# Performance work log

Measured on AMD Instinct MI355X. Metric: run time of the kernel, lower is better.

Reference implementation:

```python
import jax, jax.numpy as jnp
import numpy as np
from jax import lax

B, T, I, H = 4096, 128, 16, 64


def setup_inputs() -> dict:
    key = jax.random.key(0)
    ks = jax.random.split(key, 7)
    s_ih = 1.0 / np.sqrt(H)
    return {
        "x": jax.random.normal(ks[0], (B, T, I), dtype=jnp.float32),
        "w_ih": jax.random.uniform(ks[1], (3 * H, I), jnp.float32, -s_ih, s_ih),
        "w_hh": jax.random.uniform(ks[2], (3 * H, H), jnp.float32, -s_ih, s_ih),
        "b_ih": jax.random.uniform(ks[3], (3 * H,), jnp.float32, -s_ih, s_ih),
        "b_hh": jax.random.uniform(ks[4], (3 * H,), jnp.float32, -s_ih, s_ih),
        "fc_w": jax.random.uniform(ks[5], (1, H), jnp.float32, -s_ih, s_ih),
        "fc_b": jax.random.uniform(ks[6], (1,), jnp.float32, -s_ih, s_ih),
    }


def reference(x, w_ih, w_hh, b_ih, b_hh, fc_w, fc_b):
    # x: [B, T, I]. PyTorch GRU gate order: r, z, n.
    # Precompute input contributions to all gates for all timesteps: [B, T, 3H]
    xg = jnp.einsum('bti,gi->btg', x, w_ih) + b_ih

    def step(h, xg_t):
        # xg_t: [B, 3H], h: [B, H]
        gi_r, gi_z, gi_n = jnp.split(xg_t, 3, axis=-1)
        hg = h @ w_hh.T + b_hh  # [B, 3H]
        hr, hz, hn = jnp.split(hg, 3, axis=-1)
        r = jax.nn.sigmoid(gi_r + hr)
        z = jax.nn.sigmoid(gi_z + hz)
        n = jnp.tanh(gi_n + r * hn)
        h_new = (1.0 - z) * n + z * h
        return h_new, None

    h0 = jnp.zeros((x.shape[0], w_hh.shape[1]), dtype=x.dtype)
    hT, _ = lax.scan(step, h0, jnp.swapaxes(xg, 0, 1))  # scan over time

    # Final-step linear head, squeeze to [B]
    pred = hT @ fc_w.T + fc_b  # [B, 1]
    return pred.squeeze(-1)
```

## Files before the change

### kernel.cpp

```cpp
#include <hip/hip_runtime.h>
#include <stdint.h>


#define T_STEPS 128
#define NI 16
#define NH 64
#define RB 16

typedef float    f32x4  __attribute__((ext_vector_type(4)));
typedef uint32_t u32x4  __attribute__((ext_vector_type(4)));
typedef uint32_t u32x2  __attribute__((ext_vector_type(2)));
typedef short    bf16x8 __attribute__((ext_vector_type(8)));
typedef __bf16   bfv8   __attribute__((ext_vector_type(8)));

static constexpr float LOG2E = 1.4426950408889634f;

static __device__ __forceinline__ uint32_t fbits(float f) { return __builtin_bit_cast(uint32_t, f); }
static __device__ __forceinline__ float    bitsf(uint32_t u) { return __builtin_bit_cast(float, u); }

static __device__ __forceinline__ bf16x8 ld_frag16(const unsigned char* p) {
  u32x4 v = *(const u32x4*)p;
  return __builtin_bit_cast(bf16x8, v);
}

#define MFMA(A, B, C) __builtin_amdgcn_mfma_f32_16x16x32_bf16(A, B, C, 0, 0, 0)

static __device__ __forceinline__ bf16x8 pack_xfrag(f32x4 xa, f32x4 xb, bool hi_grp) {
  float v[8];
  #pragma unroll
  for (int j = 0; j < 4; ++j) {
    float x0 = xa[j], x1 = xb[j];
    float b0 = bitsf(fbits(x0) & 0xffff0000u);
    float b1 = bitsf(fbits(x1) & 0xffff0000u);
    v[j]     = hi_grp ? x0 : (x0 - b0);
    v[4 + j] = hi_grp ? x1 : (x1 - b1);
  }
  uint32_t d0 = __builtin_amdgcn_perm(fbits(v[1]), fbits(v[0]), 0x07060302u);
  uint32_t d1 = __builtin_amdgcn_perm(fbits(v[3]), fbits(v[2]), 0x07060302u);
  uint32_t d2 = __builtin_amdgcn_perm(fbits(v[5]), fbits(v[4]), 0x07060302u);
  uint32_t d3 = __builtin_amdgcn_perm(fbits(v[7]), fbits(v[6]), 0x07060302u);
  u32x4 u = {d0, d1, d2, d3};
  return __builtin_bit_cast(bf16x8, u);
}

__global__ __launch_bounds__(256)
void gru_fused(const float* __restrict__ x,
               const float* __restrict__ w_ih,
               const float* __restrict__ w_hh,
               const float* __restrict__ b_ih,
               const float* __restrict__ b_hh,
               const float* __restrict__ fc_w,
               const float* __restrict__ fc_b,
               float* __restrict__ out)
{
  __shared__ __align__(16) unsigned char sH[2][2][2048];
  __shared__ float s_red[4][16];

  const int tid  = threadIdx.x;
  const int lane = tid & 63;
  const int wv   = tid >> 6;
  const int colg = lane & 15;
  const int grp  = lane >> 4;
  const int rb   = blockIdx.x * RB;
  const int hc   = wv * 16 + colg;

  {
    uint32_t* p = (uint32_t*)sH;
    #pragma unroll
    for (int i = 0; i < 8; ++i) p[tid + 256 * i] = 0u;
  }

  const float scl0 = -LOG2E, scl2 = 2.0f * LOG2E;
  bf16x8 whi[3][2], wlo[3][2], axw[3];
  #pragma unroll
  for (int g = 0; g < 3; ++g) {
    const float s = (g == 2) ? scl2 : scl0;
    const float* wr = w_hh + (size_t)(g * 64 + hc) * NH + grp * 8;
    #pragma unroll
    for (int kt = 0; kt < 2; ++kt) {
      bfv8 vhi, vlo;
      #pragma unroll
      for (int j = 0; j < 8; ++j) {
        float w = wr[kt * 32 + j] * s;
        __bf16 hi = (__bf16)w;
        vhi[j] = hi;
        vlo[j] = (__bf16)(w - (float)hi);
      }
      whi[g][kt] = __builtin_bit_cast(bf16x8, vhi);
      wlo[g][kt] = __builtin_bit_cast(bf16x8, vlo);
    }
    const float* wi = w_ih + (size_t)(g * 64 + hc) * NI + (grp & 1) * 8;
    bfv8 vx;
    #pragma unroll
    for (int j = 0; j < 8; ++j) vx[j] = (__bf16)(wi[j] * s);
    axw[g] = __builtin_bit_cast(bf16x8, vx);
  }

  f32x4 bR4, bZ4, bNh4, bNx4;
  #pragma unroll
  for (int q = 0; q < 4; ++q) {
    const int hx = wv * 16 + grp * 4 + q;
    bR4[q]  = scl0 * (b_ih[hx] + b_hh[hx]);
    bZ4[q]  = scl0 * (b_ih[64 + hx] + b_hh[64 + hx]);
    bNh4[q] = scl2 * b_hh[128 + hx];
    bNx4[q] = scl2 * b_ih[128 + hx];
  }

  const int swz = colg & 7;
  const int rd0 = colg * 128 + ((0 + grp) ^ swz) * 16;
  const int rd1 = colg * 128 + ((4 + grp) ^ swz) * 16;
  const int wrh = colg * 128 + ((wv * 2 + (grp >> 1)) ^ swz) * 16 + (grp & 1) * 8;

  float hreg[4] = {0.f, 0.f, 0.f, 0.f};

  const float* xp = x + (size_t)(rb + colg) * T_STEPS * NI + (grp & 1) * 8;
  const bool hi_grp = (grp < 2);
  bf16x8 xf = pack_xfrag(*(const f32x4*)xp, *(const f32x4*)(xp + 4), hi_grp);

  const f32x4 zz = {0.f, 0.f, 0.f, 0.f};

  __syncthreads();

  for (int t = 0; t < T_STEPS; ++t) {
    const unsigned char* rb_hi = &sH[t & 1][0][0];
    const unsigned char* rb_lo = &sH[t & 1][1][0];
    bf16x8 hi0 = ld_frag16(rb_hi + rd0);
    bf16x8 hi1 = ld_frag16(rb_hi + rd1);
    bf16x8 lo0 = ld_frag16(rb_lo + rd0);
    bf16x8 lo1 = ld_frag16(rb_lo + rd1);

    const int tn = (t < T_STEPS - 1) ? (t + 1) : t;
    f32x4 xna = *(const f32x4*)(xp + (size_t)tn * NI);
    f32x4 xnb = *(const f32x4*)(xp + (size_t)tn * NI + 4);

    f32x4 cR1 = MFMA(axw[0], xf, bR4);
    f32x4 cZ1 = MFMA(axw[1], xf, bZ4);
    f32x4 aNx = MFMA(axw[2], xf, bNx4);
    f32x4 cR2 = MFMA(whi[0][1], lo1, zz);
    f32x4 cZ2 = MFMA(whi[1][1], lo1, zz);
    f32x4 cN2 = MFMA(whi[2][1], lo1, zz);
    f32x4 cN1 = MFMA(whi[2][0], hi0, bNh4);
    cR1 = MFMA(whi[0][0], hi0, cR1); cZ1 = MFMA(whi[1][0], hi0, cZ1);
    cR2 = MFMA(wlo[0][0], hi0, cR2); cZ2 = MFMA(wlo[1][0], hi0, cZ2);
    cN2 = MFMA(wlo[2][0], hi0, cN2);
    cN1 = MFMA(whi[2][1], hi1, cN1);
    cR1 = MFMA(whi[0][1], hi1, cR1); cZ1 = MFMA(whi[1][1], hi1, cZ1);
    cR2 = MFMA(wlo[0][1], hi1, cR2); cZ2 = MFMA(wlo[1][1], hi1, cZ2);
    cN2 = MFMA(wlo[2][1], hi1, cN2);
    cN1 = MFMA(whi[2][0], lo0, cN1);
    cR1 = MFMA(whi[0][0], lo0, cR1); cZ1 = MFMA(whi[1][0], lo0, cZ1);

    f32x4 aR = cR1 + cR2;
    f32x4 aZ = cZ1 + cZ2;

    float eR0 = __builtin_amdgcn_exp2f(aR[0]), eR1 = __builtin_amdgcn_exp2f(aR[1]);
    float eR2 = __builtin_amdgcn_exp2f(aR[2]), eR3 = __builtin_amdgcn_exp2f(aR[3]);
    float eZ0 = __builtin_amdgcn_exp2f(aZ[0]), eZ1 = __builtin_amdgcn_exp2f(aZ[1]);
    float eZ2 = __builtin_amdgcn_exp2f(aZ[2]), eZ3 = __builtin_amdgcn_exp2f(aZ[3]);

    f32x4 aNh = cN1 + cN2;

    bf16x8 xf_n = pack_xfrag(xna, xnb, hi_grp);

    float eRq[4] = {eR0, eR1, eR2, eR3};
    float eZq[4] = {eZ0, eZ1, eZ2, eZ3};
    float h[4];
    #pragma unroll
    for (int q = 0; q < 4; ++q) {
      float r = __builtin_amdgcn_rcpf(1.0f + eRq[q]);
      float z = __builtin_amdgcn_rcpf(1.0f + eZq[q]);
      float n = fmaf(-2.0f, __builtin_amdgcn_rcpf(
                    __builtin_amdgcn_exp2f(fmaf(r, aNh[q], aNx[q])) + 1.0f), 1.0f);
      h[q] = n + z * (hreg[q] - n);
      hreg[q] = h[q];
    }

    {
      unsigned char* wb_hi = &sH[(t + 1) & 1][0][0];
      unsigned char* wb_lo = &sH[(t + 1) & 1][1][0];
      uint32_t hi01 = __builtin_amdgcn_perm(fbits(h[1]), fbits(h[0]), 0x07060302u);
      uint32_t hi23 = __builtin_amdgcn_perm(fbits(h[3]), fbits(h[2]), 0x07060302u);
      float l0 = h[0] - bitsf(fbits(h[0]) & 0xffff0000u);
      float l1 = h[1] - bitsf(fbits(h[1]) & 0xffff0000u);
      float l2 = h[2] - bitsf(fbits(h[2]) & 0xffff0000u);
      float l3 = h[3] - bitsf(fbits(h[3]) & 0xffff0000u);
      uint32_t lo01 = __builtin_amdgcn_perm(fbits(l1), fbits(l0), 0x07060302u);
      uint32_t lo23 = __builtin_amdgcn_perm(fbits(l3), fbits(l2), 0x07060302u);
      u32x2 whiv = {hi01, hi23};
      u32x2 wlov = {lo01, lo23};
      *(u32x2*)(wb_hi + wrh) = whiv;
      *(u32x2*)(wb_lo + wrh) = wlov;
    }
    __syncthreads();
    xf = xf_n;
  }

  float s;
  {
    const int hx = wv * 16 + grp * 4;
    s = hreg[0] * fc_w[hx] + hreg[1] * fc_w[hx + 1]
      + hreg[2] * fc_w[hx + 2] + hreg[3] * fc_w[hx + 3];
  }
  s += __shfl_xor(s, 16, 64);
  s += __shfl_xor(s, 32, 64);
  if (lane < 16) s_red[wv][lane] = s;
  __syncthreads();
  if (tid < 16) {
    out[rb + tid] = s_red[0][tid] + s_red[1][tid] + s_red[2][tid] + s_red[3][tid]
                  + fc_b[0];
  }
}

extern "C" void kernel_launch(void* const* d_in, const int* in_sizes, int n_in,
                              void* d_out, int out_size, void* d_ws, size_t ws_size,
                              hipStream_t stream) {
  (void)in_sizes; (void)n_in; (void)d_ws; (void)ws_size;
  const float* x    = (const float*)d_in[0];
  const float* w_ih = (const float*)d_in[1];
  const float* w_hh = (const float*)d_in[2];
  const float* b_ih = (const float*)d_in[3];
  const float* b_hh = (const float*)d_in[4];
  const float* fc_w = (const float*)d_in[5];
  const float* fc_b = (const float*)d_in[6];
  float* out = (float*)d_out;
  const int nblocks = out_size / RB;
  gru_fused<<<dim3(nblocks), dim3(256), 0, stream>>>(x, w_ih, w_hh, b_ih, b_hh,
                                                     fc_w, fc_b, out);
}
```

Baseline: 179.3 us.

## Prefetch x two steps ahead, chain MFMAs per gate, use lighter barrier

Loads x two timesteps ahead so the global-memory latency is hidden across a full iteration, and packs the next x fragment after the h write. Each gate's MFMA chain becomes a single serial accumulation instead of two split accumulators that were summed afterward. __syncthreads is replaced by an explicit lgkmcnt wait plus s_barrier, which avoids waiting on outstanding vector-memory loads. The single-chain MFMAs lengthen each gate's dependency chain, although the three gates can still interleave.

```diff
diff --git a/kernel.cpp b/kernel.cpp
--- a/kernel.cpp
+++ b/kernel.cpp
@@ -115,13 +115,18 @@
 
   const float* xp = x + (size_t)(rb + colg) * T_STEPS * NI + (grp & 1) * 8;
   const bool hi_grp = (grp < 2);
+
   bf16x8 xf = pack_xfrag(*(const f32x4*)xp, *(const f32x4*)(xp + 4), hi_grp);
-
-  const f32x4 zz = {0.f, 0.f, 0.f, 0.f};
+  f32x4 x1a = *(const f32x4*)(xp + NI);
+  f32x4 x1b = *(const f32x4*)(xp + NI + 4);
 
   __syncthreads();
 
   for (int t = 0; t < T_STEPS; ++t) {
+    const int tn2 = (t < T_STEPS - 2) ? (t + 2) : (T_STEPS - 1);
+    f32x4 x2a = *(const f32x4*)(xp + (size_t)tn2 * NI);
+    f32x4 x2b = *(const f32x4*)(xp + (size_t)tn2 * NI + 4);
+
     const unsigned char* rb_hi = &sH[t & 1][0][0];
     const unsigned char* rb_lo = &sH[t & 1][1][0];
     bf16x8 hi0 = ld_frag16(rb_hi + rd0);
@@ -129,46 +134,28 @@
     bf16x8 lo0 = ld_frag16(rb_lo + rd0);
     bf16x8 lo1 = ld_frag16(rb_lo + rd1);
 
-    const int tn = (t < T_STEPS - 1) ? (t + 1) : t;
-    f32x4 xna = *(const f32x4*)(xp + (size_t)tn * NI);
-    f32x4 xnb = *(const f32x4*)(xp + (size_t)tn * NI + 4);
-
-    f32x4 cR1 = MFMA(axw[0], xf, bR4);
-    f32x4 cZ1 = MFMA(axw[1], xf, bZ4);
+    f32x4 aR  = MFMA(axw[0], xf, bR4);
+    f32x4 aZ  = MFMA(axw[1], xf, bZ4);
     f32x4 aNx = MFMA(axw[2], xf, bNx4);
-    f32x4 cR2 = MFMA(whi[0][1], lo1, zz);
-    f32x4 cZ2 = MFMA(whi[1][1], lo1, zz);
-    f32x4 cN2 = MFMA(whi[2][1], lo1, zz);
-    f32x4 cN1 = MFMA(whi[2][0], hi0, bNh4);
-    cR1 = MFMA(whi[0][0], hi0, cR1); cZ1 = MFMA(whi[1][0], hi0, cZ1);
-    cR2 = MFMA(wlo[0][0], hi0, cR2); cZ2 = MFMA(wlo[1][0], hi0, cZ2);
-    cN2 = MFMA(wlo[2][0], hi0, cN2);
-    cN1 = MFMA(whi[2][1], hi1, cN1);
-    cR1 = MFMA(whi[0][1], hi1, cR1); cZ1 = MFMA(whi[1][1], hi1, cZ1);
-    cR2 = MFMA(wlo[0][1], hi1, cR2); cZ2 = MFMA(wlo[1][1], hi1, cZ2);
-    cN2 = MFMA(wlo[2][1], hi1, cN2);
-    cN1 = MFMA(whi[2][0], lo0, cN1);
-    cR1 = MFMA(whi[0][0], lo0, cR1); cZ1 = MFMA(whi[1][0], lo0, cZ1);
-
-    f32x4 aR = cR1 + cR2;
-    f32x4 aZ = cZ1 + cZ2;
-
-    float eR0 = __builtin_amdgcn_exp2f(aR[0]), eR1 = __builtin_amdgcn_exp2f(aR[1]);
-    float eR2 = __builtin_amdgcn_exp2f(aR[2]), eR3 = __builtin_amdgcn_exp2f(aR[3]);
-    float eZ0 = __builtin_amdgcn_exp2f(aZ[0]), eZ1 = __builtin_amdgcn_exp2f(aZ[1]);
-    float eZ2 = __builtin_amdgcn_exp2f(aZ[2]), eZ3 = __builtin_amdgcn_exp2f(aZ[3]);
-
-    f32x4 aNh = cN1 + cN2;
-
-    bf16x8 xf_n = pack_xfrag(xna, xnb, hi_grp);
-
-    float eRq[4] = {eR0, eR1, eR2, eR3};
-    float eZq[4] = {eZ0, eZ1, eZ2, eZ3};
+
+    aR = MFMA(whi[0][0], hi0, aR); aR = MFMA(whi[0][1], hi1, aR);
+    aR = MFMA(whi[0][0], lo0, aR); aR = MFMA(whi[0][1], lo1, aR);
+    aR = MFMA(wlo[0][0], hi0, aR); aR = MFMA(wlo[0][1], hi1, aR);
+
+    aZ = MFMA(whi[1][0], hi0, aZ); aZ = MFMA(whi[1][1], hi1, aZ);
+    aZ = MFMA(whi[1][0], lo0, aZ); aZ = MFMA(whi[1][1], lo1, aZ);
+    aZ = MFMA(wlo[1][0], hi0, aZ); aZ = MFMA(wlo[1][1], hi1, aZ);
+
+    f32x4 aNh = MFMA(whi[2][0], hi0, bNh4);
+    aNh = MFMA(whi[2][1], hi1, aNh);
+    aNh = MFMA(whi[2][0], lo0, aNh); aNh = MFMA(whi[2][1], lo1, aNh);
+    aNh = MFMA(wlo[2][0], hi0, aNh); aNh = MFMA(wlo[2][1], hi1, aNh);
+
     float h[4];
     #pragma unroll
     for (int q = 0; q < 4; ++q) {
-      float r = __builtin_amdgcn_rcpf(1.0f + eRq[q]);
-      float z = __builtin_amdgcn_rcpf(1.0f + eZq[q]);
+      float r = __builtin_amdgcn_rcpf(1.0f + __builtin_amdgcn_exp2f(aR[q]));
+      float z = __builtin_amdgcn_rcpf(1.0f + __builtin_amdgcn_exp2f(aZ[q]));
       float n = fmaf(-2.0f, __builtin_amdgcn_rcpf(
                     __builtin_amdgcn_exp2f(fmaf(r, aNh[q], aNx[q])) + 1.0f), 1.0f);
       h[q] = n + z * (hreg[q] - n);
@@ -191,8 +178,13 @@
       *(u32x2*)(wb_hi + wrh) = whiv;
       *(u32x2*)(wb_lo + wrh) = wlov;
     }
-    __syncthreads();
-    xf = xf_n;
+
+    xf = pack_xfrag(x1a, x1b, hi_grp);
+
+    asm volatile("s_waitcnt lgkmcnt(0)" ::: "memory");
+    __builtin_amdgcn_s_barrier();
+
+    x1a = x2a; x1b = x2b;
   }
 
   float s;
```

Result: faster. 148.6 us (-17.1%).
